# Kernel tuning notes

Hardware: AMD Instinct MI355X
Metric: run time of the kernel (lower is better)

Reference implementation:

```python
import jax, jax.numpy as jnp
import numpy as np

L, S, B, E, H, M = 1024, 1024, 4, 1024, 16, 256
HD = E // H


def embed_rotary(x, cos, sin):
    # x: (B, T, E); interleaved rotary as in RotaryPositionEncoding.embed_rotary
    x2 = jnp.stack([-x[..., 1::2], x[..., ::2]], axis=-1).reshape(x.shape)
    return x * cos + x2 * sin


def setup_inputs() -> dict:
    key = jax.random.key(0)
    ks = jax.random.split(key, 12)
    return {
        "query": jax.random.normal(ks[0], (L, B, E), jnp.float32),
        "key": jax.random.normal(ks[1], (S, B, E), jnp.float32),
        "value": jax.random.normal(ks[2], (S, B, E), jnp.float32),
        "in_proj_weight": jax.random.normal(ks[3], (3 * E, E), jnp.float32) * (E ** -0.5),
        "in_proj_bias": jax.random.normal(ks[4], (3 * E,), jnp.float32) * 0.02,
        "out_proj_weight": jax.random.normal(ks[5], (E, E), jnp.float32) * (E ** -0.5),
        "out_proj_bias": jax.random.normal(ks[6], (E,), jnp.float32) * 0.02,
        "q_pe": jax.random.uniform(ks[7], (B, L, E, 2), jnp.float32),
        "kv_pe": jax.random.uniform(ks[8], (B, S, E, 2), jnp.float32),
        "k_mem": jax.random.normal(ks[9], (M, B, E), jnp.float32),
        "v_mem": jax.random.normal(ks[10], (M, B, E), jnp.float32),
        "gate_attn": jax.random.normal(ks[11], (H,), jnp.float32),
    }


def reference(query, key, value, in_proj_weight, in_proj_bias, out_proj_weight,
              out_proj_bias, q_pe, kv_pe, k_mem, v_mem, gate_attn):
    scaling = HD ** -0.5
    # separate q/k/v projections from slices of in_proj (q!=k!=v branch)
    q = query @ in_proj_weight[:E].T + in_proj_bias[:E]
    k = key @ in_proj_weight[E:2 * E].T + in_proj_bias[E:2 * E]
    v = value @ in_proj_weight[2 * E:].T + in_proj_bias[2 * E:]
    q = q * scaling
    # rotary PE applied on (B, T, E) layout
    q = embed_rotary(q.swapaxes(0, 1), q_pe[..., 0], q_pe[..., 1]).swapaxes(0, 1)
    k = embed_rotary(k.swapaxes(0, 1), kv_pe[..., 0], kv_pe[..., 1]).swapaxes(0, 1)
    # (T, B, E) -> (B*H, T, HD)
    qh = q.reshape(L, B * H, HD).swapaxes(0, 1)
    kh = k.reshape(S, B * H, HD).swapaxes(0, 1)
    vh = v.reshape(S, B * H, HD).swapaxes(0, 1)
    scores = jnp.einsum('bld,bsd->bls', qh, kh)  # (B*H, L, S)
    # slot-competition: softmax over queries, renormalize over keys
    w = jax.nn.softmax(scores, axis=-2) + 1e-8
    w = w / jnp.sum(w, axis=-1, keepdims=True)
    attn = jnp.einsum('bls,bsd->bld', w, vh)
    # memory attention (k_mem/v_mem already projected, shape (M, B, E))
    kmh = k_mem.reshape(M, B * H, HD).swapaxes(0, 1)
    vmh = v_mem.reshape(M, B * H, HD).swapaxes(0, 1)
    wm = jax.nn.softmax(jnp.einsum('bld,bmd->blm', qh, kmh), axis=-1)
    attn_mem = jnp.einsum('blm,bmd->bld', wm, vmh)
    # per-head sigmoid gating between memory and main outputs
    gate = jnp.tile(jax.nn.sigmoid(gate_attn), B)[:, None, None]  # (B*H,1,1)
    attn = gate * attn_mem + (1.0 - gate) * attn
    out = attn.swapaxes(0, 1).reshape(L, B, E) @ out_proj_weight.T + out_proj_bias
    return out
```

## Files before the change

kernel.cpp:

```cpp
#include <hip/hip_runtime.h>
#include <hip/hip_bf16.h>

typedef __bf16 bf16;
typedef __bf16 bf16x8 __attribute__((ext_vector_type(8)));
typedef float f32x4 __attribute__((ext_vector_type(4)));

#define LL 1024
#define SS 1024
#define BB 4
#define EE 1024
#define HH 16
#define MM 256
#define HD 64
#define BH 64

__device__ __forceinline__ f32x4 mfma16(bf16x8 a, bf16x8 b, f32x4 c) {
  return __builtin_amdgcn_mfma_f32_16x16x32_bf16(a, b, c, 0, 0, 0);
}

__device__ __forceinline__ void gload_lds16(const bf16* g, bf16* l) {
  __builtin_amdgcn_global_load_lds(
      (const __attribute__((address_space(1))) unsigned int*)(g),
      (__attribute__((address_space(3))) unsigned int*)(l), 16, 0, 0);
}

__device__ __forceinline__ bf16x8 cvt8(const float* p) {
  const f32x4 lo = *reinterpret_cast<const f32x4*>(p);
  const f32x4 hi = *reinterpret_cast<const f32x4*>(p + 4);
  bf16x8 r;
  r[0] = (bf16)lo[0]; r[1] = (bf16)lo[1]; r[2] = (bf16)lo[2]; r[3] = (bf16)lo[3];
  r[4] = (bf16)hi[0]; r[5] = (bf16)hi[1]; r[6] = (bf16)hi[2]; r[7] = (bf16)hi[3];
  return r;
}

__global__ __launch_bounds__(256) void cvt_all_kernel(
    const float* __restrict__ ipw, const float* __restrict__ opw,
    const float* __restrict__ k_mem, const float* __restrict__ query,
    const float* __restrict__ key_i, const float* __restrict__ value,
    bf16* __restrict__ wb, bf16* __restrict__ opwb, bf16* __restrict__ kmemb,
    bf16* __restrict__ xq, bf16* __restrict__ xk, bf16* __restrict__ xv) {
  const int bid = blockIdx.x, tid = threadIdx.x;
  if (bid >= 6656) {
    const size_t i8 = ((size_t)(bid - 6656) * 256 + tid) * 8;
    const int e = (int)(i8 & (EE - 1));
    const int row = (int)(i8 >> 10);
    const int s = row >> 2, b = row & 3;
    *reinterpret_cast<bf16x8*>(xv + (((size_t)b * SS + s) << 10) + e) = cvt8(value + i8);
    return;
  }
  const float* src; bf16* dst; int base;
  if (bid < 1536)      { src = ipw;   dst = wb;    base = 0; }
  else if (bid < 2048) { src = opw;   dst = opwb;  base = 1536; }
  else if (bid < 2560) { src = k_mem; dst = kmemb; base = 2048; }
  else if (bid < 4608) { src = query; dst = xq;    base = 2560; }
  else                 { src = key_i; dst = xk;    base = 4608; }
  const size_t i = ((size_t)(bid - base) * 256 + tid) * 8;
  *reinterpret_cast<bf16x8*>(dst + i) = cvt8(src + i);
}

__global__ __launch_bounds__(256) void vmt_kernel(
    const float* __restrict__ v_mem, bf16* __restrict__ vmT) {
  __shared__ float sm[64][65];
  const int bid = blockIdx.x;
  const int bh = bid >> 2, mc = bid & 3;
  const int b = bh >> 4, h = bh & 15;
  const int m0 = mc * 64;
  const int tid = threadIdx.x;
  const int d = tid & 63, mi = tid >> 6;
#pragma unroll
  for (int mm = mi; mm < 64; mm += 4)
    sm[mm][d] = v_mem[((size_t)(m0 + mm) * BB + b) * EE + h * 64 + d];
  __syncthreads();
  const int mw = tid & 63, di = tid >> 6;
#pragma unroll
  for (int dd = di; dd < 64; dd += 4)
    vmT[((size_t)bh * HD + dd) * MM + m0 + mw] = (bf16)sm[mw][dd];
}

__global__ __launch_bounds__(256) void rope_kernel(
    bf16* __restrict__ qh, bf16* __restrict__ kh,
    const float* __restrict__ q_pe, const float* __restrict__ kv_pe) {
  const size_t CP = (size_t)BH * LL * HD / 8;
  size_t gi = (size_t)blockIdx.x * 256 + threadIdx.x;
  bf16* x; const float* pe;
  if (gi < CP) { x = qh; pe = q_pe; }
  else         { x = kh; pe = kv_pe; gi -= CP; }
  const int d8 = gi & 7;
  const int t  = (int)((gi >> 3) & (LL - 1));
  const int bh = (int)(gi >> 13);
  const int b = bh >> 4, h = bh & 15;
  bf16* xp = x + gi * 8;
  const float* pp = pe + (((size_t)b * LL + t) * EE + h * 64 + d8 * 8) * 2;
  bf16x8 v = *reinterpret_cast<const bf16x8*>(xp);
  const f32x4 p0 = *reinterpret_cast<const f32x4*>(pp);
  const f32x4 p1 = *reinterpret_cast<const f32x4*>(pp + 4);
  const f32x4 p2 = *reinterpret_cast<const f32x4*>(pp + 8);
  const f32x4 p3 = *reinterpret_cast<const f32x4*>(pp + 12);
  float cs[8], sn[8], xv[8];
  cs[0]=p0[0]; sn[0]=p0[1]; cs[1]=p0[2]; sn[1]=p0[3];
  cs[2]=p1[0]; sn[2]=p1[1]; cs[3]=p1[2]; sn[3]=p1[3];
  cs[4]=p2[0]; sn[4]=p2[1]; cs[5]=p2[2]; sn[5]=p2[3];
  cs[6]=p3[0]; sn[6]=p3[1]; cs[7]=p3[2]; sn[7]=p3[3];
#pragma unroll
  for (int j = 0; j < 8; ++j) xv[j] = (float)v[j];
  bf16x8 o;
#pragma unroll
  for (int j = 0; j < 8; j += 2) {
    o[j]     = (bf16)(xv[j]     * cs[j]     - xv[j + 1] * sn[j]);
    o[j + 1] = (bf16)(xv[j + 1] * cs[j + 1] + xv[j]     * sn[j + 1]);
  }
  *reinterpret_cast<bf16x8*>(xp) = o;
}

__global__ __launch_bounds__(256) void gemm3_kernel(
    const bf16* __restrict__ xq, const bf16* __restrict__ xk,
    const bf16* __restrict__ xv, const bf16* __restrict__ wb,
    const float* __restrict__ ipb, bf16* __restrict__ qh,
    bf16* __restrict__ kh, bf16* __restrict__ vhT) {
  __shared__ bf16 As[2][4096];
  __shared__ bf16 Bs[2][4096];
  const int tid = threadIdx.x;
  const int wv = tid >> 6, lane = tid & 63;
  const int lrow = lane & 15, lkg = lane >> 4;
  const int wr = wv >> 1, wc = wv & 1;
  const int n = (blockIdx.x & 7) * 96 + (blockIdx.x >> 3);
  const int which = n >> 8, sub = n & 255;

  const bf16* X; const bf16* W;
  int rowA0, colB0;
  if (which == 2) {
    X = wb + 2 * (size_t)EE * EE;
    W = xv;
    rowA0 = (sub & 7) * 128;
    colB0 = (sub >> 3) * 128;
  } else {
    X = (which == 0) ? xq : xk;
    W = wb + (size_t)which * EE * EE;
    rowA0 = (sub >> 3) * 128;
    colB0 = (sub & 7) * 128;
  }

  const f32x4 zero = {0.f, 0.f, 0.f, 0.f};
  f32x4 acc[4][4];
#pragma unroll
  for (int i = 0; i < 4; ++i)
#pragma unroll
    for (int j = 0; j < 4; ++j) acc[i][j] = zero;

  auto stage = [&](int buf, int k0) {
#pragma unroll
    for (int t = 0; t < 2; ++t) {
      const int i = wv * 2 + t;
      const int slot = i * 64 + lane;
      const int srow = slot & 127, sk8 = slot >> 7;
      gload_lds16(X + (size_t)(rowA0 + srow) * EE + k0 + sk8 * 8, &As[buf][i * 512]);
      gload_lds16(W + (size_t)(colB0 + srow) * EE + k0 + sk8 * 8, &Bs[buf][i * 512]);
    }
  };

  stage(0, 0);
  __syncthreads();
  for (int ks = 0; ks < 32; ++ks) {
    const int buf = ks & 1;
    if (ks < 31) stage(buf ^ 1, (ks + 1) * 32);
    bf16x8 av[4], bv[4];
#pragma unroll
    for (int i = 0; i < 4; ++i) {
      av[i] = *reinterpret_cast<const bf16x8*>(&As[buf][lkg * 1024 + (wr * 64 + i * 16 + lrow) * 8]);
      bv[i] = *reinterpret_cast<const bf16x8*>(&Bs[buf][lkg * 1024 + (wc * 64 + i * 16 + lrow) * 8]);
    }
#pragma unroll
    for (int mt = 0; mt < 4; ++mt)
#pragma unroll
      for (int nt = 0; nt < 4; ++nt)
        acc[mt][nt] = mfma16(av[mt], bv[nt], acc[mt][nt]);
    __syncthreads();
  }

  if (which == 2) {
#pragma unroll
    for (int mt = 0; mt < 4; ++mt) {
#pragma unroll
      for (int r = 0; r < 4; ++r) {
        const int rowg = rowA0 + wr * 64 + mt * 16 + lkg * 4 + r;
        const float bs = ipb[2 * EE + rowg];
        const int h = rowg >> 6, d = rowg & 63;
#pragma unroll
        for (int nt = 0; nt < 4; ++nt) {
          const int c = colB0 + wc * 64 + nt * 16 + lrow;
          const int b = c >> 10, s = c & (SS - 1);
          vhT[(((size_t)(b * HH + h)) * HD + d) * SS + s] = (bf16)(acc[mt][nt][r] + bs);
        }
      }
    }
  } else {
#pragma unroll
    for (int nt = 0; nt < 4; ++nt) {
      const int col = colB0 + wc * 64 + nt * 16 + lrow;
      const float bs = ipb[which * EE + col];
      const int h = col >> 6, d = col & 63;
#pragma unroll
      for (int mt = 0; mt < 4; ++mt) {
#pragma unroll
        for (int r = 0; r < 4; ++r) {
          const int rowg = rowA0 + wr * 64 + mt * 16 + lkg * 4 + r;
          const int t = rowg >> 2;
          const int b = rowg & 3;
          float v = acc[mt][nt][r] + bs;
          if (which == 0) v *= 0.125f;
          const int bh = b * HH + h;
          if (which == 1)
            kh[((size_t)bh * LL + t) * HD + d] = (bf16)v;
          else
            qh[((size_t)bh * LL + t) * HD + d] = (bf16)v;
        }
      }
    }
  }
}

__global__ __launch_bounds__(256) void gemm_out_kernel(
    const bf16* __restrict__ Xb, const bf16* __restrict__ W,
    const float* __restrict__ bias, float* __restrict__ outf) {
  __shared__ bf16 As[2][4096];
  __shared__ bf16 Bs[2][2048];
  const int tid = threadIdx.x;
  const int wv = tid >> 6, lane = tid & 63;
  const int lrow = lane & 15, lkg = lane >> 4;
  const int wr = wv >> 1, wc = wv & 1;
  const int n = (blockIdx.x & 7) * 64 + (blockIdx.x >> 3);
  const int rowt = n >> 4, colt = n & 15;
  const int rowA0 = rowt * 128, colB0 = colt * 64;

  const f32x4 zero = {0.f, 0.f, 0.f, 0.f};
  f32x4 acc[4][2];
#pragma unroll
  for (int i = 0; i < 4; ++i)
#pragma unroll
    for (int j = 0; j < 2; ++j) acc[i][j] = zero;

  auto stage = [&](int buf, int k0) {
#pragma unroll
    for (int t = 0; t < 2; ++t) {
      const int i = wv * 2 + t;
      const int slot = i * 64 + lane;
      const int srow = slot & 127, sk8 = slot >> 7;
      gload_lds16(Xb + (size_t)(rowA0 + srow) * EE + k0 + sk8 * 8, &As[buf][i * 512]);
    }
    {
      const int slot = wv * 64 + lane;
      const int srow = slot & 63, sk8 = slot >> 6;
      gload_lds16(W + (size_t)(colB0 + srow) * EE + k0 + sk8 * 8, &Bs[buf][wv * 512]);
    }
  };

  stage(0, 0);
  __syncthreads();
  for (int ks = 0; ks < 32; ++ks) {
    const int buf = ks & 1;
    if (ks < 31) stage(buf ^ 1, (ks + 1) * 32);
    bf16x8 av[4], bv[2];
#pragma unroll
    for (int i = 0; i < 4; ++i)
      av[i] = *reinterpret_cast<const bf16x8*>(&As[buf][lkg * 1024 + (wr * 64 + i * 16 + lrow) * 8]);
#pragma unroll
    for (int j = 0; j < 2; ++j)
      bv[j] = *reinterpret_cast<const bf16x8*>(&Bs[buf][lkg * 512 + (wc * 32 + j * 16 + lrow) * 8]);
#pragma unroll
    for (int mt = 0; mt < 4; ++mt)
#pragma unroll
      for (int nt = 0; nt < 2; ++nt)
        acc[mt][nt] = mfma16(av[mt], bv[nt], acc[mt][nt]);
    __syncthreads();
  }

#pragma unroll
  for (int nt = 0; nt < 2; ++nt) {
    const int col = colB0 + wc * 32 + nt * 16 + lrow;
    const float bs = bias[col];
#pragma unroll
    for (int mt = 0; mt < 4; ++mt)
#pragma unroll
      for (int r = 0; r < 4; ++r) {
        const int rowg = rowA0 + wr * 64 + mt * 16 + lkg * 4 + r;
        outf[(size_t)rowg * EE + col] = acc[mt][nt][r] + bs;
      }
  }
}

__global__ __launch_bounds__(256) void stats_kernel(
    const bf16* __restrict__ qh, const bf16* __restrict__ kh,
    float* __restrict__ moff) {
  __shared__ float sm[4][4][16], sd[4][4][16];
  const int tid = threadIdx.x;
  const int wv = tid >> 6, lane = tid & 63;
  const int lrow = lane & 15, lkg = lane >> 4;
  const int n = blockIdx.x;
  const int j = n >> 3;
  const int bh = (n & 7) + 8 * (j >> 4);
  const int s0 = (j & 15) * 64;

  bf16x8 b0[4], b1[4];
#pragma unroll
  for (int ct = 0; ct < 4; ++ct) {
    const bf16* kp = kh + ((size_t)bh * SS + s0 + ct * 16 + lrow) * HD + lkg * 8;
    b0[ct] = *reinterpret_cast<const bf16x8*>(kp);
    b1[ct] = *reinterpret_cast<const bf16x8*>(kp + 32);
  }

  const f32x4 zero = {0.f, 0.f, 0.f, 0.f};
  float m[4] = {-1e30f, -1e30f, -1e30f, -1e30f};
  float d[4] = {0.f, 0.f, 0.f, 0.f};
  const bf16* qbase = qh + ((size_t)bh * LL + wv * 256 + lrow) * HD + lkg * 8;
  for (int i = 0; i < 16; ++i) {
    bf16x8 a0 = *reinterpret_cast<const bf16x8*>(qbase + (size_t)i * 16 * HD);
    bf16x8 a1 = *reinterpret_cast<const bf16x8*>(qbase + (size_t)i * 16 * HD + 32);
#pragma unroll
    for (int ct = 0; ct < 4; ++ct) {
      f32x4 c = zero;
      c = mfma16(a0, b0[ct], c);
      c = mfma16(a1, b1[ct], c);
      float tm = fmaxf(fmaxf(c[0], c[1]), fmaxf(c[2], c[3]));
      float nm = fmaxf(m[ct], tm);
      float dd = d[ct] * __expf(m[ct] - nm);
#pragma unroll
      for (int r = 0; r < 4; ++r) dd += __expf(c[r] - nm);
      d[ct] = dd; m[ct] = nm;
    }
  }
#pragma unroll
  for (int off = 16; off < 64; off <<= 1) {
#pragma unroll
    for (int ct = 0; ct < 4; ++ct) {
      float mo = __shfl_xor(m[ct], off);
      float dd = __shfl_xor(d[ct], off);
      float nm = fmaxf(m[ct], mo);
      d[ct] = d[ct] * __expf(m[ct] - nm) + dd * __expf(mo - nm);
      m[ct] = nm;
    }
  }
  if (lkg == 0) {
#pragma unroll
    for (int ct = 0; ct < 4; ++ct) { sm[wv][ct][lrow] = m[ct]; sd[wv][ct][lrow] = d[ct]; }
  }
  __syncthreads();
  if (wv == 0 && lkg == 0) {
#pragma unroll
    for (int ct = 0; ct < 4; ++ct) {
      float mm = sm[0][ct][lrow], dd = sd[0][ct][lrow];
#pragma unroll
      for (int w = 1; w < 4; ++w) {
        float mo = sm[w][ct][lrow], d2 = sd[w][ct][lrow];
        float nm = fmaxf(mm, mo);
        dd = dd * __expf(mm - nm) + d2 * __expf(mo - nm);
        mm = nm;
      }
      moff[(size_t)bh * SS + s0 + ct * 16 + lrow] = mm + __logf(dd);
    }
  }
}

__global__ __launch_bounds__(64) void colsum_kernel(
    const bf16* __restrict__ vhT, float* __restrict__ colsum) {
  const int bh = blockIdx.x, d = blockIdx.y, lane = threadIdx.x;
  const bf16* p = vhT + ((size_t)bh * HD + d) * SS;
  float s = 0.f;
  for (int i = lane; i < SS; i += 64) s += (float)p[i];
#pragma unroll
  for (int off = 32; off; off >>= 1) s += __shfl_xor(s, off);
  if (lane == 0) colsum[bh * HD + d] = s;
}

__global__ __launch_bounds__(256) void attn_kernel(
    const bf16* __restrict__ qh, const bf16* __restrict__ kh,
    const bf16* __restrict__ vhT, const bf16* __restrict__ vmT,
    const bf16* __restrict__ k_mem, const float* __restrict__ gate_w,
    const float* __restrict__ moff, const float* __restrict__ colsum,
    bf16* __restrict__ attn2) {
  __shared__ bf16 Ks[2][2048];
  __shared__ bf16 Vs[2][2048];
  __shared__ bf16 wt[4][32][40];
  const int tid = threadIdx.x;
  const int wv = tid >> 6, lane = tid & 63;
  const int lrow = lane & 15, lkg = lane >> 4;
  const int bid = blockIdx.x;
  const int bh = (bid & 7) + 8 * (bid >> 6);
  const int b = bh >> 4, h = bh & 15;
  const int l0 = ((bid >> 3) & 7) * 128 + wv * 32;

  bf16x8 aq[2][2];
#pragma unroll
  for (int rt = 0; rt < 2; ++rt) {
    const bf16* qp = qh + ((size_t)bh * LL + l0 + rt * 16 + lrow) * HD + lkg * 8;
    aq[rt][0] = *reinterpret_cast<const bf16x8*>(qp);
    aq[rt][1] = *reinterpret_cast<const bf16x8*>(qp + 32);
  }

  bf16x8 ones;
#pragma unroll
  for (int i = 0; i < 8; ++i) ones[i] = (bf16)1.0f;

  const f32x4 zero = {0.f, 0.f, 0.f, 0.f};
  f32x4 acc[2][4], accm[2][4], racc[2];
#pragma unroll
  for (int rt = 0; rt < 2; ++rt) {
    racc[rt] = zero;
#pragma unroll
    for (int i = 0; i < 4; ++i) { acc[rt][i] = zero; accm[rt][i] = zero; }
  }

  const int srow = lane & 31, sk8h = lane >> 5;
  auto stageK = [&](int buf, int s0) {
    gload_lds16(kh + ((size_t)bh * SS + s0 + srow) * HD + (wv * 2 + sk8h) * 8,
                &Ks[buf][wv * 512]);
  };
  auto stageV = [&](int buf, int s0) {
    gload_lds16(vhT + ((size_t)bh * HD + lane) * SS + s0 + wv * 8,
                &Vs[buf][wv * 512]);
  };
  auto stageKM = [&](int buf, int m0) {
    gload_lds16(k_mem + ((size_t)(m0 + srow) * BB + b) * EE + h * 64 + (wv * 2 + sk8h) * 8,
                &Ks[buf][wv * 512]);
  };
  auto stageVM = [&](int buf, int m0) {
    gload_lds16(vmT + ((size_t)bh * HD + lane) * MM + m0 + wv * 8,
                &Vs[buf][wv * 512]);
  };
  auto kfrag = [&](int buf, int t, int half) {
    return *reinterpret_cast<const bf16x8*>(&Ks[buf][((half * 4 + lkg) * 32 + t * 16 + lrow) * 8]);
  };
  auto vfrag = [&](int buf, int dt) {
    return *reinterpret_cast<const bf16x8*>(&Vs[buf][(lkg * 64 + dt * 16 + lrow) * 8]);
  };

  stageK(0, 0); stageV(0, 0);
  __syncthreads();
  for (int s0 = 0; s0 < SS; s0 += 32) {
    const int buf = (s0 >> 5) & 1;
    if (s0 + 32 < SS) { stageK(buf ^ 1, s0 + 32); stageV(buf ^ 1, s0 + 32); }
    bf16x8 kf[2][2];
#pragma unroll
    for (int t = 0; t < 2; ++t) { kf[t][0] = kfrag(buf, t, 0); kf[t][1] = kfrag(buf, t, 1); }
    f32x4 sc[2][2];
#pragma unroll
    for (int rt = 0; rt < 2; ++rt)
#pragma unroll
      for (int t = 0; t < 2; ++t) {
        f32x4 c = zero;
        c = mfma16(aq[rt][0], kf[t][0], c);
        c = mfma16(aq[rt][1], kf[t][1], c);
        sc[rt][t] = c;
      }
#pragma unroll
    for (int t = 0; t < 2; ++t) {
      const float mo = moff[(size_t)bh * SS + s0 + t * 16 + lrow];
#pragma unroll
      for (int rt = 0; rt < 2; ++rt)
#pragma unroll
        for (int r = 0; r < 4; ++r)
          wt[wv][rt * 16 + lkg * 4 + r][t * 16 + lrow] = (bf16)__expf(sc[rt][t][r] - mo);
    }
    bf16x8 aw[2];
#pragma unroll
    for (int rt = 0; rt < 2; ++rt) {
      aw[rt] = *reinterpret_cast<const bf16x8*>(&wt[wv][rt * 16 + lrow][lkg * 8]);
      racc[rt] = mfma16(aw[rt], ones, racc[rt]);
    }
#pragma unroll
    for (int dt = 0; dt < 4; ++dt) {
      bf16x8 bv = vfrag(buf, dt);
#pragma unroll
      for (int rt = 0; rt < 2; ++rt) acc[rt][dt] = mfma16(aw[rt], bv, acc[rt][dt]);
    }
    __syncthreads();
  }

  float mx[2][4], dn[2][4];
#pragma unroll
  for (int rt = 0; rt < 2; ++rt)
#pragma unroll
    for (int r = 0; r < 4; ++r) { mx[rt][r] = -1e30f; dn[rt][r] = 0.f; }
  stageKM(0, 0);
  __syncthreads();
  for (int m0 = 0; m0 < MM; m0 += 32) {
    const int buf = (m0 >> 5) & 1;
    if (m0 + 32 < MM) stageKM(buf ^ 1, m0 + 32);
    bf16x8 kf[2][2];
#pragma unroll
    for (int t = 0; t < 2; ++t) { kf[t][0] = kfrag(buf, t, 0); kf[t][1] = kfrag(buf, t, 1); }
#pragma unroll
    for (int rt = 0; rt < 2; ++rt)
#pragma unroll
      for (int t = 0; t < 2; ++t) {
        f32x4 c = zero;
        c = mfma16(aq[rt][0], kf[t][0], c);
        c = mfma16(aq[rt][1], kf[t][1], c);
#pragma unroll
        for (int r = 0; r < 4; ++r) {
          float nm = fmaxf(mx[rt][r], c[r]);
          dn[rt][r] = dn[rt][r] * __expf(mx[rt][r] - nm) + __expf(c[r] - nm);
          mx[rt][r] = nm;
        }
      }
    __syncthreads();
  }
#pragma unroll
  for (int off = 1; off < 16; off <<= 1) {
#pragma unroll
    for (int rt = 0; rt < 2; ++rt)
#pragma unroll
      for (int r = 0; r < 4; ++r) {
        float mo = __shfl_xor(mx[rt][r], off);
        float dd = __shfl_xor(dn[rt][r], off);
        float nm = fmaxf(mx[rt][r], mo);
        dn[rt][r] = dn[rt][r] * __expf(mx[rt][r] - nm) + dd * __expf(mo - nm);
        mx[rt][r] = nm;
      }
  }
#pragma unroll
  for (int rt = 0; rt < 2; ++rt)
#pragma unroll
    for (int r = 0; r < 4; ++r) dn[rt][r] = 1.f / dn[rt][r];

  stageKM(0, 0); stageVM(0, 0);
  __syncthreads();
  for (int m0 = 0; m0 < MM; m0 += 32) {
    const int buf = (m0 >> 5) & 1;
    if (m0 + 32 < MM) { stageKM(buf ^ 1, m0 + 32); stageVM(buf ^ 1, m0 + 32); }
    bf16x8 kf[2][2];
#pragma unroll
    for (int t = 0; t < 2; ++t) { kf[t][0] = kfrag(buf, t, 0); kf[t][1] = kfrag(buf, t, 1); }
#pragma unroll
    for (int rt = 0; rt < 2; ++rt)
#pragma unroll
      for (int t = 0; t < 2; ++t) {
        f32x4 c = zero;
        c = mfma16(aq[rt][0], kf[t][0], c);
        c = mfma16(aq[rt][1], kf[t][1], c);
#pragma unroll
        for (int r = 0; r < 4; ++r)
          wt[wv][rt * 16 + lkg * 4 + r][t * 16 + lrow] = (bf16)(__expf(c[r] - mx[rt][r]) * dn[rt][r]);
      }
    bf16x8 aw[2];
#pragma unroll
    for (int rt = 0; rt < 2; ++rt)
      aw[rt] = *reinterpret_cast<const bf16x8*>(&wt[wv][rt * 16 + lrow][lkg * 8]);
#pragma unroll
    for (int dt = 0; dt < 4; ++dt) {
      bf16x8 bv = vfrag(buf, dt);
#pragma unroll
      for (int rt = 0; rt < 2; ++rt) accm[rt][dt] = mfma16(aw[rt], bv, accm[rt][dt]);
    }
    __syncthreads();
  }

  float g = gate_w[h];
  g = 1.f / (1.f + __expf(-g));

#pragma unroll
  for (int dt = 0; dt < 4; ++dt) {
    const int d = dt * 16 + lrow;
    const float cv = colsum[bh * HD + d] * 1e-8f;
#pragma unroll
    for (int rt = 0; rt < 2; ++rt)
#pragma unroll
      for (int r = 0; r < 4; ++r) {
        const int lg = l0 + rt * 16 + lkg * 4 + r;
        const float den = racc[rt][r] + (float)SS * 1e-8f;
        const float amain = (acc[rt][dt][r] + cv) / den;
        const float v = g * accm[rt][dt][r] + (1.f - g) * amain;
        attn2[((size_t)lg * BB + b) * EE + h * 64 + d] = (bf16)v;
      }
  }
}

extern "C" void kernel_launch(void* const* d_in, const int* in_sizes, int n_in,
                              void* d_out, int out_size, void* d_ws, size_t ws_size,
                              hipStream_t stream) {
  const float* query = (const float*)d_in[0];
  const float* key_i = (const float*)d_in[1];
  const float* value = (const float*)d_in[2];
  const float* ipw   = (const float*)d_in[3];
  const float* ipb   = (const float*)d_in[4];
  const float* opw   = (const float*)d_in[5];
  const float* opb   = (const float*)d_in[6];
  const float* q_pe  = (const float*)d_in[7];
  const float* kv_pe = (const float*)d_in[8];
  const float* k_mem = (const float*)d_in[9];
  const float* v_mem = (const float*)d_in[10];
  const float* gate  = (const float*)d_in[11];

  char* ws = (char*)d_ws;
  bf16* qh    = (bf16*)(ws);
  bf16* kh    = (bf16*)(ws + (8u << 20));
  bf16* vhT   = (bf16*)(ws + (16u << 20));
  bf16* attn2 = (bf16*)(ws + (24u << 20));
  bf16* vmT   = (bf16*)(ws + (32u << 20));
  float* moff   = (float*)(ws + (34u << 20));
  float* colsum = (float*)(ws + (34u << 20) + (1u << 18));
  bf16* wb    = (bf16*)(ws + (35u << 20));
  bf16* opwb  = (bf16*)(ws + (41u << 20));
  bf16* kmemb = (bf16*)(ws + (43u << 20));
  bf16* xq = attn2;
  bf16* xk = (bf16*)d_out;
  bf16* xv = (bf16*)d_out + (size_t)SS * BB * EE;

  dim3 blk(256);
  hipLaunchKernelGGL(cvt_all_kernel, dim3(8704), blk, 0, stream, ipw, opw, k_mem,
                     query, key_i, value, wb, opwb, kmemb, xq, xk, xv);
  hipLaunchKernelGGL(vmt_kernel, dim3(256), blk, 0, stream, v_mem, vmT);
  hipLaunchKernelGGL(gemm3_kernel, dim3(768), blk, 0, stream, xq, xk, xv, wb,
                     ipb, qh, kh, vhT);
  hipLaunchKernelGGL(rope_kernel, dim3(4096), blk, 0, stream, qh, kh, q_pe, kv_pe);
  hipLaunchKernelGGL(stats_kernel, dim3(1024), blk, 0, stream, qh, kh, moff);
  hipLaunchKernelGGL(colsum_kernel, dim3(64, 64), dim3(64), 0, stream, vhT, colsum);
  hipLaunchKernelGGL(attn_kernel, dim3(512), blk, 0, stream, qh, kh, vhT, vmT,
                     kmemb, gate, moff, colsum, attn2);
  hipLaunchKernelGGL(gemm_out_kernel, dim3(512), blk, 0, stream, attn2, opwb, opb,
                     (float*)d_out);
}
```

Measured before the change: 226.9 us.

## Switch GEMM and attention loops to triple-buffered LDS ring with partial vmcnt waits

Replaces double buffering with a three-slot LDS ring in the projection GEMMs, output GEMM and attention main/memory loops, so each tile is prefetched two iterations ahead. The full __syncthreads is replaced by an s_waitcnt vmcnt(N) plus s_barrier that waits only for the older batch of global-to-LDS loads, letting the newest batch stay in flight across the barrier. This aims to hide global-load latency better, at the cost of more shared memory per block (possibly lower occupancy). It also relies on the vmcnt counts exactly matching the number of loads issued per stage.

```diff
diff --git a/kernel.cpp b/kernel.cpp
--- a/kernel.cpp
+++ b/kernel.cpp
@@ -23,6 +23,13 @@
       (const __attribute__((address_space(1))) unsigned int*)(g),
       (__attribute__((address_space(3))) unsigned int*)(l), 16, 0, 0);
 }
+
+#define RING_BARRIER(N)                                         \
+  do {                                                          \
+    asm volatile("s_waitcnt vmcnt(" #N ")" ::: "memory");       \
+    __builtin_amdgcn_s_barrier();                               \
+    __builtin_amdgcn_sched_barrier(0);                          \
+  } while (0)
 
 __device__ __forceinline__ bf16x8 cvt8(const float* p) {
   const f32x4 lo = *reinterpret_cast<const f32x4*>(p);
@@ -117,8 +124,8 @@
     const bf16* __restrict__ xv, const bf16* __restrict__ wb,
     const float* __restrict__ ipb, bf16* __restrict__ qh,
     bf16* __restrict__ kh, bf16* __restrict__ vhT) {
-  __shared__ bf16 As[2][4096];
-  __shared__ bf16 Bs[2][4096];
+  __shared__ bf16 As[3][4096];
+  __shared__ bf16 Bs[3][4096];
   const int tid = threadIdx.x;
   const int wv = tid >> 6, lane = tid & 63;
   const int lrow = lane & 15, lkg = lane >> 4;
@@ -159,10 +166,11 @@
   };
 
   stage(0, 0);
-  __syncthreads();
+  stage(1, 32);
+  RING_BARRIER(4);
   for (int ks = 0; ks < 32; ++ks) {
-    const int buf = ks & 1;
-    if (ks < 31) stage(buf ^ 1, (ks + 1) * 32);
+    const int buf = ks % 3;
+    if (ks + 2 < 32) stage((ks + 2) % 3, (ks + 2) * 32);
     bf16x8 av[4], bv[4];
 #pragma unroll
     for (int i = 0; i < 4; ++i) {
@@ -174,7 +182,7 @@
 #pragma unroll
       for (int nt = 0; nt < 4; ++nt)
         acc[mt][nt] = mfma16(av[mt], bv[nt], acc[mt][nt]);
-    __syncthreads();
+    if (ks + 2 < 32) { RING_BARRIER(4); } else { RING_BARRIER(0); }
   }
 
   if (which == 2) {
@@ -222,8 +230,8 @@
 __global__ __launch_bounds__(256) void gemm_out_kernel(
     const bf16* __restrict__ Xb, const bf16* __restrict__ W,
     const float* __restrict__ bias, float* __restrict__ outf) {
-  __shared__ bf16 As[2][4096];
-  __shared__ bf16 Bs[2][2048];
+  __shared__ bf16 As[3][4096];
+  __shared__ bf16 Bs[3][2048];
   const int tid = threadIdx.x;
   const int wv = tid >> 6, lane = tid & 63;
   const int lrow = lane & 15, lkg = lane >> 4;
@@ -255,10 +263,11 @@
   };
 
   stage(0, 0);
-  __syncthreads();
+  stage(1, 32);
+  RING_BARRIER(3);
   for (int ks = 0; ks < 32; ++ks) {
-    const int buf = ks & 1;
-    if (ks < 31) stage(buf ^ 1, (ks + 1) * 32);
+    const int buf = ks % 3;
+    if (ks + 2 < 32) stage((ks + 2) % 3, (ks + 2) * 32);
     bf16x8 av[4], bv[2];
 #pragma unroll
     for (int i = 0; i < 4; ++i)
@@ -271,7 +280,7 @@
 #pragma unroll
       for (int nt = 0; nt < 2; ++nt)
         acc[mt][nt] = mfma16(av[mt], bv[nt], acc[mt][nt]);
-    __syncthreads();
+    if (ks + 2 < 32) { RING_BARRIER(3); } else { RING_BARRIER(0); }
   }
 
 #pragma unroll
@@ -377,8 +386,8 @@
     const bf16* __restrict__ k_mem, const float* __restrict__ gate_w,
     const float* __restrict__ moff, const float* __restrict__ colsum,
     bf16* __restrict__ attn2) {
-  __shared__ bf16 Ks[2][2048];
-  __shared__ bf16 Vs[2][2048];
+  __shared__ bf16 Ks[3][2048];
+  __shared__ bf16 Vs[3][2048];
   __shared__ bf16 wt[4][32][40];
   const int tid = threadIdx.x;
   const int wv = tid >> 6, lane = tid & 63;
@@ -434,10 +443,12 @@
   };
 
   stageK(0, 0); stageV(0, 0);
-  __syncthreads();
+  stageK(1, 32); stageV(1, 32);
+  RING_BARRIER(2);
   for (int s0 = 0; s0 < SS; s0 += 32) {
-    const int buf = (s0 >> 5) & 1;
-    if (s0 + 32 < SS) { stageK(buf ^ 1, s0 + 32); stageV(buf ^ 1, s0 + 32); }
+    const int idx = s0 >> 5;
+    const int buf = idx % 3;
+    if (s0 + 64 < SS) { stageK((idx + 2) % 3, s0 + 64); stageV((idx + 2) % 3, s0 + 64); }
     bf16x8 kf[2][2];
 #pragma unroll
     for (int t = 0; t < 2; ++t) { kf[t][0] = kfrag(buf, t, 0); kf[t][1] = kfrag(buf, t, 1); }
@@ -472,7 +483,7 @@
 #pragma unroll
       for (int rt = 0; rt < 2; ++rt) acc[rt][dt] = mfma16(aw[rt], bv, acc[rt][dt]);
     }
-    __syncthreads();
+    if (s0 + 64 < SS) { RING_BARRIER(2); } else { RING_BARRIER(0); }
   }
 
   float mx[2][4], dn[2][4];
@@ -481,10 +492,12 @@
 #pragma unroll
     for (int r = 0; r < 4; ++r) { mx[rt][r] = -1e30f; dn[rt][r] = 0.f; }
   stageKM(0, 0);
-  __syncthreads();
+  stageKM(1, 32);
+  RING_BARRIER(1);
   for (int m0 = 0; m0 < MM; m0 += 32) {
-    const int buf = (m0 >> 5) & 1;
-    if (m0 + 32 < MM) stageKM(buf ^ 1, m0 + 32);
+    const int idx = m0 >> 5;
+    const int buf = idx % 3;
+    if (m0 + 64 < MM) stageKM((idx + 2) % 3, m0 + 64);
     bf16x8 kf[2][2];
 #pragma unroll
     for (int t = 0; t < 2; ++t) { kf[t][0] = kfrag(buf, t, 0); kf[t][1] = kfrag(buf, t, 1); }
@@ -502,7 +515,7 @@
           mx[rt][r] = nm;
         }
       }
-    __syncthreads();
+    if (m0 + 64 < MM) { RING_BARRIER(1); } else { RING_BARRIER(0); }
   }
 #pragma unroll
   for (int off = 1; off < 16; off <<= 1) {
@@ -523,10 +536,12 @@
     for (int r = 0; r < 4; ++r) dn[rt][r] = 1.f / dn[rt][r];
 
   stageKM(0, 0); stageVM(0, 0);
-  __syncthreads();
+  stageKM(1, 32); stageVM(1, 32);
+  RING_BARRIER(2);
   for (int m0 = 0; m0 < MM; m0 += 32) {
-    const int buf = (m0 >> 5) & 1;
-    if (m0 + 32 < MM) { stageKM(buf ^ 1, m0 + 32); stageVM(buf ^ 1, m0 + 32); }
+    const int idx = m0 >> 5;
+    const int buf = idx % 3;
+    if (m0 + 64 < MM) { stageKM((idx + 2) % 3, m0 + 64); stageVM((idx + 2) % 3, m0 + 64); }
     bf16x8 kf[2][2];
 #pragma unroll
     for (int t = 0; t < 2; ++t) { kf[t][0] = kfrag(buf, t, 0); kf[t][1] = kfrag(buf, t, 1); }
@@ -551,7 +566,7 @@
 #pragma unroll
       for (int rt = 0; rt < 2; ++rt) accm[rt][dt] = mfma16(aw[rt], bv, accm[rt][dt]);
     }
-    __syncthreads();
+    if (m0 + 64 < MM) { RING_BARRIER(2); } else { RING_BARRIER(0); }
   }
 
   float g = gate_w[h];
```

Result: no change. 227.8 us (+0.4%).
